# Performance work log

Measured on AMD Instinct MI355X. Metric: run time of the kernel, lower is better.

The kernel has to match this reference:

```python
import itertools
import jax, jax.numpy as jnp
import numpy as np

B, N, F = 128, 128, 64  # batch, n_nodes, feat

def _edge_indices(n_nodes, receiving=True):
    # itertools.permutations(range(n), 2) ordering, matching the original layer
    pairs = np.array(list(itertools.permutations(range(n_nodes), 2)), dtype=np.int32)
    return pairs[:, 0] if receiving else pairs[:, 1]  # [n_edges]

def setup_inputs() -> dict:
    key = jax.random.key(0)
    x = jax.random.normal(key, (B, N, F), dtype=jnp.float32)
    return {"x": x}

def reference(x) -> jnp.ndarray:
    # node_to_edge=True, receiving=True: adjacency[0, i, r]=1 selects receiver node
    # of edge i; dense matmul A @ x is exactly a gather x[:, idx, :].
    n_nodes = x.shape[-2]
    idx = jnp.asarray(_edge_indices(n_nodes, receiving=True))  # [n_edges]
    return jnp.take(x, idx, axis=-2)  # [B, n_edges, F]
```

## Files before the change

kernel.cpp:

```cpp
#include <hip/hip_runtime.h>


constexpr unsigned Bn  = 128;
constexpr unsigned Nn  = 128;
constexpr unsigned Fn  = 64;
constexpr unsigned NE  = Nn * (Nn - 1);
constexpr unsigned F4  = Fn / 4;
constexpr unsigned TOTAL4 = Bn * NE * F4;

__global__ __launch_bounds__(256) void node_edge_gather(
    const float4* __restrict__ x, float4* __restrict__ out) {
    unsigned stride = gridDim.x * blockDim.x;
    for (unsigned o = blockIdx.x * blockDim.x + threadIdx.x; o < TOTAL4; o += stride) {
        unsigned f4   = o & (F4 - 1);
        unsigned rest = o >> 4;
        unsigned e    = rest % NE;
        unsigned b    = rest / NE;
        unsigned node = e / (Nn - 1);
        out[o] = x[(b * Nn + node) * F4 + f4];
    }
}

extern "C" void kernel_launch(void* const* d_in, const int* in_sizes, int n_in,
                              void* d_out, int out_size, void* d_ws, size_t ws_size,
                              hipStream_t stream) {
    const float4* x = (const float4*)d_in[0];
    float4* out = (float4*)d_out;

    unsigned threads = 256;
    unsigned blocks = (TOTAL4 + threads - 1) / threads;
    if (blocks > 2048) blocks = 2048;

    node_edge_gather<<<blocks, threads, 0, stream>>>(x, out);
}
```

Baseline: 117.2 us.

## Broadcast each node row to its edges with one block per node

Replaces the grid-stride gather, which did integer divides and modulos on every output element, with one block per (batch, node). Each block loads its node's 64-float row once and writes it to that node's 127 contiguous edge rows using nontemporal stores. This removes the per-element index arithmetic and the redundant reloads of x, and the nontemporal hint is meant to keep the large write stream out of the caches. Launching 16384 blocks instead of a capped 2048 adds some block scheduling overhead.

Result: faster. 103.1 us (-12.0%).

```diff
diff --git a/kernel.cpp b/kernel.cpp
--- a/kernel.cpp
+++ b/kernel.cpp
@@ -1,35 +1,38 @@
 #include <hip/hip_runtime.h>
 
 
-constexpr unsigned Bn  = 128;
-constexpr unsigned Nn  = 128;
-constexpr unsigned Fn  = 64;
-constexpr unsigned NE  = Nn * (Nn - 1);
-constexpr unsigned F4  = Fn / 4;
-constexpr unsigned TOTAL4 = Bn * NE * F4;
+typedef float f32x4 __attribute__((ext_vector_type(4)));
 
-__global__ __launch_bounds__(256) void node_edge_gather(
-    const float4* __restrict__ x, float4* __restrict__ out) {
-    unsigned stride = gridDim.x * blockDim.x;
-    for (unsigned o = blockIdx.x * blockDim.x + threadIdx.x; o < TOTAL4; o += stride) {
-        unsigned f4   = o & (F4 - 1);
-        unsigned rest = o >> 4;
-        unsigned e    = rest % NE;
-        unsigned b    = rest / NE;
-        unsigned node = e / (Nn - 1);
-        out[o] = x[(b * Nn + node) * F4 + f4];
+constexpr unsigned Bn = 128;
+constexpr unsigned Nn = 128;
+constexpr unsigned Fn = 64;
+constexpr unsigned NE = Nn * (Nn - 1);
+constexpr unsigned F4 = Fn / 4;
+
+__global__ __launch_bounds__(256) void node_edge_bcast(
+    const f32x4* __restrict__ x, f32x4* __restrict__ out) {
+    const unsigned blk  = blockIdx.x;
+    const unsigned tid  = threadIdx.x;
+    const unsigned f4   = tid & (F4 - 1);
+    const unsigned row0 = tid >> 4;
+
+    const f32x4 v = x[blk * F4 + f4];
+
+    const unsigned b    = blk >> 7;
+    const unsigned node = blk & (Nn - 1);
+    f32x4* dst = out + (b * NE + node * (Nn - 1)) * F4;
+
+    #pragma unroll
+    for (unsigned r = row0; r < Nn - 1; r += 16) {
+        __builtin_nontemporal_store(v, &dst[r * F4 + f4]);
     }
 }
 
 extern "C" void kernel_launch(void* const* d_in, const int* in_sizes, int n_in,
                               void* d_out, int out_size, void* d_ws, size_t ws_size,
                               hipStream_t stream) {
-    const float4* x = (const float4*)d_in[0];
-    float4* out = (float4*)d_out;
+    const f32x4* x = (const f32x4*)d_in[0];
+    f32x4* out = (f32x4*)d_out;
 
-    unsigned threads = 256;
-    unsigned blocks = (TOTAL4 + threads - 1) / threads;
-    if (blocks > 2048) blocks = 2048;
-
-    node_edge_gather<<<blocks, threads, 0, stream>>>(x, out);
+    node_edge_bcast<<<Bn * Nn, 256, 0, stream>>>(x, out);
 }
```
